# Kernel tuning notes

Hardware: AMD Instinct MI355X
Metric: run time of the kernel (lower is better)

Reference implementation:

```python
import jax, jax.numpy as jnp
import numpy as np

D_MODEL = 1024
N_HEADS = 16
D_FF = 4096
HEAD_DIM = D_MODEL // N_HEADS
LN_EPS = 1e-5


def layer_norm(x, g, b):
    m = jnp.mean(x, axis=-1, keepdims=True)
    v = jnp.mean(jnp.square(x - m), axis=-1, keepdims=True)
    return (x - m) * jax.lax.rsqrt(v + LN_EPS) * g + b


def setup_inputs() -> dict:
    key = jax.random.key(0)
    ks = jax.random.split(key, 16)
    s = 0.02
    d = {
        'x': jax.random.normal(ks[0], (4, 2048, D_MODEL), jnp.float32),
        'Wq': jax.random.normal(ks[1], (D_MODEL, D_MODEL), jnp.float32) * s,
        'bq': jnp.zeros((D_MODEL,), jnp.float32),
        'Wk': jax.random.normal(ks[2], (D_MODEL, D_MODEL), jnp.float32) * s,
        'bk': jnp.zeros((D_MODEL,), jnp.float32),
        'Wv': jax.random.normal(ks[3], (D_MODEL, D_MODEL), jnp.float32) * s,
        'bv': jnp.zeros((D_MODEL,), jnp.float32),
        'Wo': jax.random.normal(ks[4], (D_MODEL, D_MODEL), jnp.float32) * s,
        'bo': jnp.zeros((D_MODEL,), jnp.float32),
        'W1': jax.random.normal(ks[5], (D_FF, D_MODEL), jnp.float32) * s,
        'b1': jnp.zeros((D_FF,), jnp.float32),
        'W2': jax.random.normal(ks[6], (D_MODEL, D_FF), jnp.float32) * s,
        'b2': jnp.zeros((D_MODEL,), jnp.float32),
        'g1': jnp.ones((D_MODEL,), jnp.float32),
        'be1': jnp.zeros((D_MODEL,), jnp.float32),
        'g2': jnp.ones((D_MODEL,), jnp.float32),
        'be2': jnp.zeros((D_MODEL,), jnp.float32),
    }
    return d


def reference(x, Wq, bq, Wk, bk, Wv, bv, Wo, bo, W1, b1, W2, b2, g1, be1, g2, be2):
    B, S, D = x.shape
    H, hd = N_HEADS, HEAD_DIM
    # QKV projections; chunk along d_model -> heads (same as reshape last dim)
    q = (x @ Wq.T + bq).reshape(B, S, H, hd)
    k = (x @ Wk.T + bk).reshape(B, S, H, hd)
    v = (x @ Wv.T + bv).reshape(B, S, H, hd)
    # scaled dot-product attention (no mask, dropout = identity in eval)
    scores = jnp.einsum('bqhd,bkhd->bhqk', q, k) / jnp.sqrt(jnp.float32(hd))
    attn = jax.nn.softmax(scores, axis=-1)
    ctx = jnp.einsum('bhqk,bkhd->bqhd', attn, v).reshape(B, S, D)
    out1 = ctx @ Wo.T + bo
    out = layer_norm(x + out1, g1, be1)
    out2 = jax.nn.relu(out @ W1.T + b1) @ W2.T + b2
    # NOTE: faithful to source bug: second residual uses out1, not out
    return layer_norm(out1 + out2, g2, be2)
```

## Files before the change

kernel.cpp:

```cpp
#include <hip/hip_runtime.h>

typedef __bf16 bf16_t;
typedef __bf16 bf16x8 __attribute__((ext_vector_type(8)));
typedef __bf16 bf16x4 __attribute__((ext_vector_type(4)));
typedef float  f32x4  __attribute__((ext_vector_type(4)));

#define SEQ   2048
#define DMODEL 1024
#define DFF   4096
#define NHEAD 16
#define HDIM  64
#define MTOK  8192

#define MB (size_t)(1024*1024)
static const size_t XB_OFF   = 0;
static const size_t Q_OFF    = 16*MB;
static const size_t K_OFF    = 32*MB;
static const size_t VT_OFF   = 48*MB;
static const size_t FFN1_OFF = 0;
static const size_t CTX_OFF  = 64*MB;
static const size_t OUT1_OFF = 80*MB;
static const size_t LN1_OFF  = 112*MB;
static const size_t WQ_OFF   = 128*MB;
static const size_t WK_OFF   = 130*MB;
static const size_t WV_OFF   = 132*MB;
static const size_t WO_OFF   = 134*MB;
static const size_t W1_OFF   = 136*MB;
static const size_t W2_OFF   = 144*MB;

__device__ inline void gload16(const void* g, void* l) {
    __builtin_amdgcn_global_load_lds((__attribute__((address_space(1))) void*)g,
                                     (__attribute__((address_space(3))) void*)l, 16, 0, 0);
}

__global__ __launch_bounds__(256) void cast_bf16_k(const float* __restrict__ s,
                                                   bf16_t* __restrict__ d, int n8) {
    int i = blockIdx.x * 256 + threadIdx.x;
    if (i >= n8) return;
    float4 v0 = ((const float4*)s)[2*i];
    float4 v1 = ((const float4*)s)[2*i+1];
    bf16x8 o;
    o[0]=(bf16_t)v0.x; o[1]=(bf16_t)v0.y; o[2]=(bf16_t)v0.z; o[3]=(bf16_t)v0.w;
    o[4]=(bf16_t)v1.x; o[5]=(bf16_t)v1.y; o[6]=(bf16_t)v1.z; o[7]=(bf16_t)v1.w;
    *(bf16x8*)(d + (size_t)i*8) = o;
}

template<int EPI>
__global__ __launch_bounds__(256, 2) void gemm_bt(
    const bf16_t* __restrict__ A, const bf16_t* __restrict__ Bm,
    const float* __restrict__ bias, void* __restrict__ out,
    const float* __restrict__ aux, int M, int N, int K, float scale)
{
    __shared__ bf16_t As[128*64];
    __shared__ bf16_t Bs[128*64];
    const int tid = threadIdx.x;
    const int l   = tid & 63;
    const int wid = tid >> 6;
    const int wm  = wid >> 1, wn = wid & 1;
    const int c16 = l & 15,   g  = l >> 4;
    const long brow = (long)blockIdx.y * 128;
    const long bcol = (long)blockIdx.x * 128;

    f32x4 acc[4][4] = {};

    const int nkt = K >> 6;
    for (int kt = 0; kt < nkt; ++kt) {
        __syncthreads();
        const bf16_t* Ag = A  + brow * K + kt*64;
        const bf16_t* Bg = Bm + bcol * K + kt*64;
#pragma unroll
        for (int c = 0; c < 4; ++c) {
            int e   = (c*256 + tid) * 8;
            int row = e >> 6;
            int col = e & 63;
            gload16(Ag + (long)row*K + col, &As[e]);
            gload16(Bg + (long)row*K + col, &Bs[e]);
        }
        __syncthreads();
#pragma unroll
        for (int kk = 0; kk < 2; ++kk) {
            bf16x8 af[4], bfr[4];
#pragma unroll
            for (int mi = 0; mi < 4; ++mi)
                af[mi] = *(const bf16x8*)&As[(wm*64 + mi*16 + c16)*64 + kk*32 + 8*g];
#pragma unroll
            for (int ni = 0; ni < 4; ++ni)
                bfr[ni] = *(const bf16x8*)&Bs[(wn*64 + ni*16 + c16)*64 + kk*32 + 8*g];
#pragma unroll
            for (int mi = 0; mi < 4; ++mi)
#pragma unroll
                for (int ni = 0; ni < 4; ++ni)
                    acc[mi][ni] = __builtin_amdgcn_mfma_f32_16x16x32_bf16(
                        af[mi], bfr[ni], acc[mi][ni], 0, 0, 0);
        }
    }

#pragma unroll
    for (int ni = 0; ni < 4; ++ni) {
        const long c = bcol + wn*64 + ni*16 + c16;
        const float bv = bias[c];
#pragma unroll
        for (int mi = 0; mi < 4; ++mi) {
#pragma unroll
            for (int i = 0; i < 4; ++i) {
                const long r = brow + wm*64 + mi*16 + g*4 + i;
                float v = (acc[mi][ni][i] + bv) * scale;
                if constexpr (EPI == 0) {
                    long off = (((r >> 11)*NHEAD + (c >> 6))*SEQ + (r & (SEQ-1)))*HDIM + (c & 63);
                    ((bf16_t*)out)[off] = (bf16_t)v;
                } else if constexpr (EPI == 1) {
                    long off = (((r >> 11)*NHEAD + (c >> 6))*HDIM + (c & 63))*SEQ + (r & (SEQ-1));
                    ((bf16_t*)out)[off] = (bf16_t)v;
                } else if constexpr (EPI == 2) {
                    ((float*)out)[r*N + c] = v;
                } else if constexpr (EPI == 3) {
                    ((bf16_t*)out)[r*N + c] = (bf16_t)fmaxf(v, 0.f);
                } else {
                    ((float*)out)[r*N + c] = v + aux[r*N + c];
                }
            }
        }
    }
}

__device__ __forceinline__ void kload(bf16x8 (&dst)[4][2], const bf16_t* kb0,
                                      int ktt, int c16, int g) {
    const bf16_t* kbase = kb0 + (size_t)ktt*64*HDIM;
#pragma unroll
    for (int j = 0; j < 4; ++j)
#pragma unroll
        for (int ks = 0; ks < 2; ++ks)
            dst[j][ks] = *(const bf16x8*)(kbase + (size_t)(4*c16 + j)*HDIM + ks*32 + 8*g);
}

__device__ __forceinline__ void vload(bf16x8 (&vr)[4][2], const bf16_t* vt0,
                                      int ktt, int c16, int g) {
#pragma unroll
    for (int nf = 0; nf < 4; ++nf)
#pragma unroll
        for (int ks = 0; ks < 2; ++ks)
            vr[nf][ks] = *(const bf16x8*)(vt0 + (size_t)(16*nf + c16)*SEQ + ktt*64 + ks*32 + 8*g);
}

__device__ __forceinline__ void attn_step(
    const bf16x8 (&kr)[4][2], const bf16x8 (&vr)[4][2], const bf16x8 (&aq)[2][2],
    f32x4 (&acc)[2][4], float (&m)[2][4], float (&ls)[2][4],
    char* myP, int c16, int g)
{
    f32x4 s[2][4];
    const f32x4 z = {0.f, 0.f, 0.f, 0.f};
#pragma unroll
    for (int f = 0; f < 2; ++f)
#pragma unroll
        for (int j = 0; j < 4; ++j) {
            s[f][j] = __builtin_amdgcn_mfma_f32_16x16x32_bf16(aq[f][0], kr[j][0], z, 0, 0, 0);
            s[f][j] = __builtin_amdgcn_mfma_f32_16x16x32_bf16(aq[f][1], kr[j][1], s[f][j], 0, 0, 0);
        }
#pragma unroll
    for (int f = 0; f < 2; ++f)
#pragma unroll
        for (int i = 0; i < 4; ++i) {
            float pm = fmaxf(fmaxf(s[f][0][i], s[f][1][i]), fmaxf(s[f][2][i], s[f][3][i]));
#pragma unroll
            for (int msk = 1; msk < 16; msk <<= 1)
                pm = fmaxf(pm, __shfl_xor(pm, msk, 64));
            float mn   = fmaxf(m[f][i], pm);
            float corr = __expf(m[f][i] - mn);
            float rsum = 0.f;
#pragma unroll
            for (int j = 0; j < 4; ++j) { s[f][j][i] = __expf(s[f][j][i] - mn); rsum += s[f][j][i]; }
#pragma unroll
            for (int msk = 1; msk < 16; msk <<= 1)
                rsum += __shfl_xor(rsum, msk, 64);
            ls[f][i] = ls[f][i]*corr + rsum;
            m[f][i]  = mn;
#pragma unroll
            for (int nf = 0; nf < 4; ++nf) acc[f][nf][i] *= corr;
        }
#pragma unroll
    for (int f = 0; f < 2; ++f)
#pragma unroll
        for (int i = 0; i < 4; ++i) {
            const int rw = f*16 + 4*g + i;
            bf16x4 pk;
            pk[0]=(bf16_t)s[f][0][i]; pk[1]=(bf16_t)s[f][1][i];
            pk[2]=(bf16_t)s[f][2][i]; pk[3]=(bf16_t)s[f][3][i];
            *(bf16x4*)(myP + rw*128 + ((8*c16) ^ ((rw & 7) << 4))) = pk;
        }
    asm volatile("s_waitcnt lgkmcnt(0)" ::: "memory");
    __builtin_amdgcn_sched_barrier(0);
#pragma unroll
    for (int f = 0; f < 2; ++f)
#pragma unroll
        for (int ks = 0; ks < 2; ++ks) {
            bf16x8 pa = *(const bf16x8*)(myP + (f*16 + c16)*128 + ((ks*64 + 16*g) ^ ((c16 & 7) << 4)));
#pragma unroll
            for (int nf = 0; nf < 4; ++nf)
                acc[f][nf] = __builtin_amdgcn_mfma_f32_16x16x32_bf16(pa, vr[nf][ks], acc[f][nf], 0, 0, 0);
        }
}

__global__ __launch_bounds__(256, 2) void attn_k(
    const bf16_t* __restrict__ qb, const bf16_t* __restrict__ kb,
    const bf16_t* __restrict__ vt, bf16_t* __restrict__ ctx)
{
    const int bh = blockIdx.y;
    const int w  = threadIdx.x >> 6;
    const int l  = threadIdx.x & 63;
    const int c16 = l & 15, g = l >> 4;
    const int q0 = blockIdx.x*128 + w*32;

    __shared__ char Ps[4*8192];
    char* myP = &Ps[w*8192];

    bf16x8 aq[2][2];
#pragma unroll
    for (int f = 0; f < 2; ++f) {
        const bf16_t* qrow = qb + ((size_t)bh*SEQ + q0 + f*16 + c16)*HDIM;
        aq[f][0] = *(const bf16x8*)(qrow + 8*g);
        aq[f][1] = *(const bf16x8*)(qrow + 32 + 8*g);
    }

    const bf16_t* kb0 = kb + (size_t)bh*SEQ*HDIM;
    const bf16_t* vt0 = vt + (size_t)bh*HDIM*SEQ;

    f32x4 acc[2][4] = {};
    float m[2][4]  = {{-1e30f,-1e30f,-1e30f,-1e30f},{-1e30f,-1e30f,-1e30f,-1e30f}};
    float ls[2][4] = {};

    bf16x8 kA[4][2], kB[4][2], vr[4][2];
    kload(kA, kb0, 0, c16, g);
    for (int kt = 0; kt < SEQ/64; kt += 2) {
        kload(kB, kb0, kt + 1, c16, g);
        vload(vr, vt0, kt, c16, g);
        attn_step(kA, vr, aq, acc, m, ls, myP + (kt & 1)*4096, c16, g);
        kload(kA, kb0, (kt + 2 < SEQ/64) ? kt + 2 : 0, c16, g);
        vload(vr, vt0, kt + 1, c16, g);
        attn_step(kB, vr, aq, acc, m, ls, myP + ((kt + 1) & 1)*4096, c16, g);
    }

    const int b = bh >> 4, h = bh & 15;
#pragma unroll
    for (int f = 0; f < 2; ++f)
#pragma unroll
        for (int i = 0; i < 4; ++i) {
            float inv = 1.0f / ls[f][i];
            long srow = q0 + f*16 + g*4 + i;
#pragma unroll
            for (int nf = 0; nf < 4; ++nf)
                ctx[((size_t)b*SEQ + srow)*DMODEL + h*HDIM + nf*16 + c16] = (bf16_t)(acc[f][nf][i]*inv);
        }
}

__global__ __launch_bounds__(256) void ln_k(
    const float* __restrict__ a, const float* __restrict__ b,
    const float* __restrict__ g, const float* __restrict__ be,
    float* __restrict__ of, bf16_t* __restrict__ ob)
{
    const long row = blockIdx.x;
    const int tid = threadIdx.x;
    float4 v = ((const float4*)(a + row*DMODEL))[tid];
    if (b) {
        float4 u = ((const float4*)(b + row*DMODEL))[tid];
        v.x += u.x; v.y += u.y; v.z += u.z; v.w += u.w;
    }
    float s = v.x + v.y + v.z + v.w;
    float q = v.x*v.x + v.y*v.y + v.z*v.z + v.w*v.w;
#pragma unroll
    for (int msk = 1; msk < 64; msk <<= 1) {
        s += __shfl_xor(s, msk, 64);
        q += __shfl_xor(q, msk, 64);
    }
    __shared__ float sb[4], qb2[4];
    int w = tid >> 6, lid = tid & 63;
    if (lid == 0) { sb[w] = s; qb2[w] = q; }
    __syncthreads();
    s = sb[0] + sb[1] + sb[2] + sb[3];
    q = qb2[0] + qb2[1] + qb2[2] + qb2[3];
    float mean = s * (1.f/1024.f);
    float var  = q * (1.f/1024.f) - mean*mean;
    float rs   = rsqrtf(var + 1e-5f);
    float4 gv = ((const float4*)g)[tid];
    float4 bv = ((const float4*)be)[tid];
    float o0 = (v.x-mean)*rs*gv.x + bv.x;
    float o1 = (v.y-mean)*rs*gv.y + bv.y;
    float o2 = (v.z-mean)*rs*gv.z + bv.z;
    float o3 = (v.w-mean)*rs*gv.w + bv.w;
    if (ob) {
        bf16x4 o; o[0]=(bf16_t)o0; o[1]=(bf16_t)o1; o[2]=(bf16_t)o2; o[3]=(bf16_t)o3;
        *(bf16x4*)(ob + row*DMODEL + tid*4) = o;
    } else {
        float4 o = make_float4(o0, o1, o2, o3);
        ((float4*)(of + row*DMODEL))[tid] = o;
    }
}

extern "C" void kernel_launch(void* const* d_in, const int* in_sizes, int n_in,
                              void* d_out, int out_size, void* d_ws, size_t ws_size,
                              hipStream_t stream)
{
    const float* x   = (const float*)d_in[0];
    const float* Wq  = (const float*)d_in[1];
    const float* bq  = (const float*)d_in[2];
    const float* Wk  = (const float*)d_in[3];
    const float* bk  = (const float*)d_in[4];
    const float* Wv  = (const float*)d_in[5];
    const float* bvv = (const float*)d_in[6];
    const float* Wo  = (const float*)d_in[7];
    const float* bo  = (const float*)d_in[8];
    const float* W1  = (const float*)d_in[9];
    const float* b1  = (const float*)d_in[10];
    const float* W2  = (const float*)d_in[11];
    const float* b2  = (const float*)d_in[12];
    const float* g1  = (const float*)d_in[13];
    const float* be1 = (const float*)d_in[14];
    const float* g2  = (const float*)d_in[15];
    const float* be2 = (const float*)d_in[16];

    char* ws = (char*)d_ws;
    bf16_t* xb   = (bf16_t*)(ws + XB_OFF);
    bf16_t* qbuf = (bf16_t*)(ws + Q_OFF);
    bf16_t* kbuf = (bf16_t*)(ws + K_OFF);
    bf16_t* vtb  = (bf16_t*)(ws + VT_OFF);
    bf16_t* ffn1 = (bf16_t*)(ws + FFN1_OFF);
    bf16_t* ctxb = (bf16_t*)(ws + CTX_OFF);
    float*  out1 = (float*)(ws + OUT1_OFF);
    bf16_t* ln1b = (bf16_t*)(ws + LN1_OFF);
    bf16_t* wqb  = (bf16_t*)(ws + WQ_OFF);
    bf16_t* wkb  = (bf16_t*)(ws + WK_OFF);
    bf16_t* wvb  = (bf16_t*)(ws + WV_OFF);
    bf16_t* wob  = (bf16_t*)(ws + WO_OFF);
    bf16_t* w1b  = (bf16_t*)(ws + W1_OFF);
    bf16_t* w2b  = (bf16_t*)(ws + W2_OFF);
    float*  dout = (float*)d_out;

    auto cast = [&](const float* s, bf16_t* d, long n) {
        int n8 = (int)(n / 8);
        cast_bf16_k<<<(n8 + 255)/256, 256, 0, stream>>>(s, d, n8);
    };
    cast(x,  xb,  (long)MTOK*DMODEL);
    cast(Wq, wqb, (long)DMODEL*DMODEL);
    cast(Wk, wkb, (long)DMODEL*DMODEL);
    cast(Wv, wvb, (long)DMODEL*DMODEL);
    cast(Wo, wob, (long)DMODEL*DMODEL);
    cast(W1, w1b, (long)DFF*DMODEL);
    cast(W2, w2b, (long)DMODEL*DFF);

    dim3 blk(256);
    gemm_bt<0><<<dim3(DMODEL/128, MTOK/128), blk, 0, stream>>>(xb, wqb, bq, qbuf, nullptr, MTOK, DMODEL, DMODEL, 0.125f);
    gemm_bt<0><<<dim3(DMODEL/128, MTOK/128), blk, 0, stream>>>(xb, wkb, bk, kbuf, nullptr, MTOK, DMODEL, DMODEL, 1.f);
    gemm_bt<1><<<dim3(DMODEL/128, MTOK/128), blk, 0, stream>>>(xb, wvb, bvv, vtb, nullptr, MTOK, DMODEL, DMODEL, 1.f);
    attn_k<<<dim3(SEQ/128, 4*NHEAD), blk, 0, stream>>>(qbuf, kbuf, vtb, ctxb);
    gemm_bt<2><<<dim3(DMODEL/128, MTOK/128), blk, 0, stream>>>(ctxb, wob, bo, out1, nullptr, MTOK, DMODEL, DMODEL, 1.f);
    ln_k<<<MTOK, blk, 0, stream>>>(x, out1, g1, be1, nullptr, ln1b);
    gemm_bt<3><<<dim3(DFF/128, MTOK/128), blk, 0, stream>>>(ln1b, w1b, b1, ffn1, nullptr, MTOK, DFF, DMODEL, 1.f);
    gemm_bt<4><<<dim3(DMODEL/128, MTOK/128), blk, 0, stream>>>(ffn1, w2b, b2, out1, out1, MTOK, DMODEL, DFF, 1.f);
    ln_k<<<MTOK, blk, 0, stream>>>(out1, nullptr, g2, be2, dout, nullptr);
}
```

Measured before the change: 587.4 us.

## Transpose score MFMA, use lazy max rescaling and setprio in attention

Computes S^T by swapping the MFMA operands, so each lane owns one query row's scores. This turns the 16-lane max/sum reductions into two cross-group shuffles and cuts per-lane softmax state to one value per fragment. It rescales the running max only when some row's max grows by more than 8 (a lazy rescale), which skips most correction exps and accumulator multiplies. It also raises wave priority around the MFMA blocks. In exchange it adds corr shuffles to remap rows into the accumulator layout, and the P write pattern to LDS changes.

```diff
diff --git a/kernel.cpp b/kernel.cpp
--- a/kernel.cpp
+++ b/kernel.cpp
@@ -127,10 +127,10 @@
                                       int ktt, int c16, int g) {
     const bf16_t* kbase = kb0 + (size_t)ktt*64*HDIM;
 #pragma unroll
-    for (int j = 0; j < 4; ++j)
+    for (int jk = 0; jk < 4; ++jk)
 #pragma unroll
         for (int ks = 0; ks < 2; ++ks)
-            dst[j][ks] = *(const bf16x8*)(kbase + (size_t)(4*c16 + j)*HDIM + ks*32 + 8*g);
+            dst[jk][ks] = *(const bf16x8*)(kbase + (size_t)(16*jk + c16)*HDIM + ks*32 + 8*g);
 }
 
 __device__ __forceinline__ void vload(bf16x8 (&vr)[4][2], const bf16_t* vt0,
@@ -144,60 +144,79 @@
 
 __device__ __forceinline__ void attn_step(
     const bf16x8 (&kr)[4][2], const bf16x8 (&vr)[4][2], const bf16x8 (&aq)[2][2],
-    f32x4 (&acc)[2][4], float (&m)[2][4], float (&ls)[2][4],
+    f32x4 (&acc)[2][4], float (&m)[2], float (&ls)[2],
     char* myP, int c16, int g)
 {
     f32x4 s[2][4];
     const f32x4 z = {0.f, 0.f, 0.f, 0.f};
-#pragma unroll
-    for (int f = 0; f < 2; ++f)
-#pragma unroll
-        for (int j = 0; j < 4; ++j) {
-            s[f][j] = __builtin_amdgcn_mfma_f32_16x16x32_bf16(aq[f][0], kr[j][0], z, 0, 0, 0);
-            s[f][j] = __builtin_amdgcn_mfma_f32_16x16x32_bf16(aq[f][1], kr[j][1], s[f][j], 0, 0, 0);
-        }
-#pragma unroll
-    for (int f = 0; f < 2; ++f)
-#pragma unroll
-        for (int i = 0; i < 4; ++i) {
-            float pm = fmaxf(fmaxf(s[f][0][i], s[f][1][i]), fmaxf(s[f][2][i], s[f][3][i]));
-#pragma unroll
-            for (int msk = 1; msk < 16; msk <<= 1)
-                pm = fmaxf(pm, __shfl_xor(pm, msk, 64));
-            float mn   = fmaxf(m[f][i], pm);
-            float corr = __expf(m[f][i] - mn);
-            float rsum = 0.f;
-#pragma unroll
-            for (int j = 0; j < 4; ++j) { s[f][j][i] = __expf(s[f][j][i] - mn); rsum += s[f][j][i]; }
-#pragma unroll
-            for (int msk = 1; msk < 16; msk <<= 1)
-                rsum += __shfl_xor(rsum, msk, 64);
-            ls[f][i] = ls[f][i]*corr + rsum;
-            m[f][i]  = mn;
-#pragma unroll
-            for (int nf = 0; nf < 4; ++nf) acc[f][nf][i] *= corr;
-        }
-#pragma unroll
-    for (int f = 0; f < 2; ++f)
-#pragma unroll
-        for (int i = 0; i < 4; ++i) {
-            const int rw = f*16 + 4*g + i;
+    __builtin_amdgcn_s_setprio(1);
+#pragma unroll
+    for (int qf = 0; qf < 2; ++qf)
+#pragma unroll
+        for (int jk = 0; jk < 4; ++jk) {
+            s[qf][jk] = __builtin_amdgcn_mfma_f32_16x16x32_bf16(kr[jk][0], aq[qf][0], z, 0, 0, 0);
+            s[qf][jk] = __builtin_amdgcn_mfma_f32_16x16x32_bf16(kr[jk][1], aq[qf][1], s[qf][jk], 0, 0, 0);
+        }
+    __builtin_amdgcn_s_setprio(0);
+#pragma unroll
+    for (int qf = 0; qf < 2; ++qf) {
+        float a0 = fmaxf(fmaxf(s[qf][0][0], s[qf][0][1]), fmaxf(s[qf][0][2], s[qf][0][3]));
+        float a1 = fmaxf(fmaxf(s[qf][1][0], s[qf][1][1]), fmaxf(s[qf][1][2], s[qf][1][3]));
+        float a2 = fmaxf(fmaxf(s[qf][2][0], s[qf][2][1]), fmaxf(s[qf][2][2], s[qf][2][3]));
+        float a3 = fmaxf(fmaxf(s[qf][3][0], s[qf][3][1]), fmaxf(s[qf][3][2], s[qf][3][3]));
+        float pm = fmaxf(fmaxf(a0, a1), fmaxf(a2, a3));
+        pm = fmaxf(pm, __shfl_xor(pm, 16, 64));
+        pm = fmaxf(pm, __shfl_xor(pm, 32, 64));
+        if (__any(pm > m[qf] + 8.0f)) {
+            float mn   = fmaxf(m[qf], pm);
+            float corr = __expf(m[qf] - mn);
+            ls[qf] *= corr;
+            m[qf]   = mn;
+            float c0 = __shfl(corr, 4*g + 0, 64);
+            float c1 = __shfl(corr, 4*g + 1, 64);
+            float c2 = __shfl(corr, 4*g + 2, 64);
+            float c3 = __shfl(corr, 4*g + 3, 64);
+#pragma unroll
+            for (int nf = 0; nf < 4; ++nf) {
+                acc[qf][nf][0] *= c0; acc[qf][nf][1] *= c1;
+                acc[qf][nf][2] *= c2; acc[qf][nf][3] *= c3;
+            }
+        }
+        float rsum = 0.f;
+#pragma unroll
+        for (int jk = 0; jk < 4; ++jk)
+#pragma unroll
+            for (int i = 0; i < 4; ++i) {
+                s[qf][jk][i] = __expf(s[qf][jk][i] - m[qf]);
+                rsum += s[qf][jk][i];
+            }
+        rsum += __shfl_xor(rsum, 16, 64);
+        rsum += __shfl_xor(rsum, 32, 64);
+        ls[qf] += rsum;
+    }
+#pragma unroll
+    for (int qf = 0; qf < 2; ++qf)
+#pragma unroll
+        for (int jk = 0; jk < 4; ++jk) {
             bf16x4 pk;
-            pk[0]=(bf16_t)s[f][0][i]; pk[1]=(bf16_t)s[f][1][i];
-            pk[2]=(bf16_t)s[f][2][i]; pk[3]=(bf16_t)s[f][3][i];
-            *(bf16x4*)(myP + rw*128 + ((8*c16) ^ ((rw & 7) << 4))) = pk;
+            pk[0]=(bf16_t)s[qf][jk][0]; pk[1]=(bf16_t)s[qf][jk][1];
+            pk[2]=(bf16_t)s[qf][jk][2]; pk[3]=(bf16_t)s[qf][jk][3];
+            *(bf16x4*)(myP + (qf*16 + c16)*128 + ((32*jk + 8*g) ^ ((c16 & 7) << 4))) = pk;
         }
     asm volatile("s_waitcnt lgkmcnt(0)" ::: "memory");
     __builtin_amdgcn_sched_barrier(0);
-#pragma unroll
-    for (int f = 0; f < 2; ++f)
+    __builtin_amdgcn_s_setprio(1);
+#pragma unroll
+    for (int qf = 0; qf < 2; ++qf)
 #pragma unroll
         for (int ks = 0; ks < 2; ++ks) {
-            bf16x8 pa = *(const bf16x8*)(myP + (f*16 + c16)*128 + ((ks*64 + 16*g) ^ ((c16 & 7) << 4)));
+            bf16x8 pa = *(const bf16x8*)(myP + (qf*16 + c16)*128 + ((ks*64 + 16*g) ^ ((c16 & 7) << 4)));
 #pragma unroll
             for (int nf = 0; nf < 4; ++nf)
-                acc[f][nf] = __builtin_amdgcn_mfma_f32_16x16x32_bf16(pa, vr[nf][ks], acc[f][nf], 0, 0, 0);
-        }
+                acc[qf][nf] = __builtin_amdgcn_mfma_f32_16x16x32_bf16(pa, vr[nf][ks], acc[qf][nf], 0, 0, 0);
+        }
+    __builtin_amdgcn_s_setprio(0);
+    asm volatile("" ::: "memory");
 }
 
 __global__ __launch_bounds__(256, 2) void attn_k(
@@ -215,18 +234,18 @@
 
     bf16x8 aq[2][2];
 #pragma unroll
-    for (int f = 0; f < 2; ++f) {
-        const bf16_t* qrow = qb + ((size_t)bh*SEQ + q0 + f*16 + c16)*HDIM;
-        aq[f][0] = *(const bf16x8*)(qrow + 8*g);
-        aq[f][1] = *(const bf16x8*)(qrow + 32 + 8*g);
+    for (int qf = 0; qf < 2; ++qf) {
+        const bf16_t* qrow = qb + ((size_t)bh*SEQ + q0 + qf*16 + c16)*HDIM;
+        aq[qf][0] = *(const bf16x8*)(qrow + 8*g);
+        aq[qf][1] = *(const bf16x8*)(qrow + 32 + 8*g);
     }
 
     const bf16_t* kb0 = kb + (size_t)bh*SEQ*HDIM;
     const bf16_t* vt0 = vt + (size_t)bh*HDIM*SEQ;
 
     f32x4 acc[2][4] = {};
-    float m[2][4]  = {{-1e30f,-1e30f,-1e30f,-1e30f},{-1e30f,-1e30f,-1e30f,-1e30f}};
-    float ls[2][4] = {};
+    float m[2]  = {-1e30f, -1e30f};
+    float ls[2] = {0.f, 0.f};
 
     bf16x8 kA[4][2], kB[4][2], vr[4][2];
     kload(kA, kb0, 0, c16, g);
@@ -241,15 +260,21 @@
 
     const int b = bh >> 4, h = bh & 15;
 #pragma unroll
-    for (int f = 0; f < 2; ++f)
-#pragma unroll
-        for (int i = 0; i < 4; ++i) {
-            float inv = 1.0f / ls[f][i];
-            long srow = q0 + f*16 + g*4 + i;
-#pragma unroll
-            for (int nf = 0; nf < 4; ++nf)
-                ctx[((size_t)b*SEQ + srow)*DMODEL + h*HDIM + nf*16 + c16] = (bf16_t)(acc[f][nf][i]*inv);
-        }
+    for (int qf = 0; qf < 2; ++qf) {
+        float i0 = 1.0f / __shfl(ls[qf], 4*g + 0, 64);
+        float i1 = 1.0f / __shfl(ls[qf], 4*g + 1, 64);
+        float i2 = 1.0f / __shfl(ls[qf], 4*g + 2, 64);
+        float i3 = 1.0f / __shfl(ls[qf], 4*g + 3, 64);
+#pragma unroll
+        for (int nf = 0; nf < 4; ++nf) {
+            long col = (size_t)h*HDIM + nf*16 + c16;
+            long rb  = (size_t)b*SEQ + q0 + qf*16 + 4*g;
+            ctx[(rb + 0)*DMODEL + col] = (bf16_t)(acc[qf][nf][0] * i0);
+            ctx[(rb + 1)*DMODEL + col] = (bf16_t)(acc[qf][nf][1] * i1);
+            ctx[(rb + 2)*DMODEL + col] = (bf16_t)(acc[qf][nf][2] * i2);
+            ctx[(rb + 3)*DMODEL + col] = (bf16_t)(acc[qf][nf][3] * i3);
+        }
+    }
 }
 
 __global__ __launch_bounds__(256) void ln_k(
```

Result: no change. 585.8 us (-0.3%).
